# Optimization experiments

Measured on AMD Instinct MI355X. Metric: run time of the kernel, lower is better.

Reference implementation:

```python
import jax, jax.numpy as jnp
import numpy as np


def _dense_image_warp(image, flow):
    """Faithful JAX port of tfa.image.dense_image_warp.

    image: [B,H,W,C] float, flow: [B,H,W,2] float (flow[...,0]=dy, flow[...,1]=dx).
    query point (y,x) = grid(y,x) - flow; bilinear interp with TFA's clamping:
    floor clipped to [0, size-2], alpha clipped to [0,1].
    """
    B, H, W, C = image.shape
    gy, gx = jnp.meshgrid(
        jnp.arange(H, dtype=flow.dtype), jnp.arange(W, dtype=flow.dtype), indexing="ij"
    )
    qy = gy[None] - flow[..., 0]  # [B,H,W]
    qx = gx[None] - flow[..., 1]

    y0f = jnp.clip(jnp.floor(qy), 0.0, H - 2)
    x0f = jnp.clip(jnp.floor(qx), 0.0, W - 2)
    ay = jnp.clip(qy - y0f, 0.0, 1.0)[..., None]  # [B,H,W,1]
    ax = jnp.clip(qx - x0f, 0.0, 1.0)[..., None]

    y0 = y0f.astype(jnp.int32)
    x0 = x0f.astype(jnp.int32)
    b = jnp.arange(B, dtype=jnp.int32)[:, None, None]

    tl = image[b, y0, x0]          # top-left  [B,H,W,C]
    tr = image[b, y0, x0 + 1]      # top-right
    bl = image[b, y0 + 1, x0]      # bottom-left
    br = image[b, y0 + 1, x0 + 1]  # bottom-right

    top = tl + ax * (tr - tl)
    bot = bl + ax * (br - bl)
    return top + ay * (bot - top)


def setup_inputs() -> dict:
    key = jax.random.key(0)
    k1, k2 = jax.random.split(key)
    B, H, W, C = 8, 1024, 768, 3
    image = jax.random.normal(k1, (B, H, W, C), dtype=jnp.float32)
    # flow magnitudes of a few pixels, typical for appearance-flow warping
    flow = jax.random.normal(k2, (B, H, W, 2), dtype=jnp.float32) * 5.0
    return {"image": image, "flow": flow}


def reference(image, flow):
    return _dense_image_warp(image, flow)
```

## Files before the change

### kernel.cpp

```cpp
#include <hip/hip_runtime.h>


constexpr int B = 8;
constexpr int H = 1024;
constexpr int W = 768;
constexpr int C = 3;

constexpr int TY = 32, TX = 32;
constexpr int WIN_ROWS = 65;
constexpr int WIN_COLS = 64;
constexpr int WSTRIDE = WIN_COLS * C;
constexpr int CHUNKS  = WIN_ROWS * (WSTRIDE / 4);
constexpr int TILES_X = W / TX;
constexpr int TILES_Y = H / TY;
constexpr int TILES_PER_B = TILES_X * TILES_Y;

constexpr int NTHREADS = 512;
constexpr int PX_PER_T = (TY * TX) / NTHREADS;

typedef float vfloat2 __attribute__((ext_vector_type(2)));
typedef float vfloat4 __attribute__((ext_vector_type(4)));
typedef float vfloat2_a4 __attribute__((ext_vector_type(2), aligned(4)));
typedef float vfloat4_a4 __attribute__((ext_vector_type(4), aligned(4)));

__global__ __launch_bounds__(NTHREADS, 6) void warp_kernel(
    const float* __restrict__ image,
    const float* __restrict__ flow,
    float* __restrict__ out)
{
    __shared__ float win[WIN_ROWS * WSTRIDE + 64];

    const int flat = blockIdx.x;
    const int b    = flat & 7;
    const int s    = flat >> 3;
    const int ty   = s / TILES_X;
    const int tx   = s - ty * TILES_X;
    const int Y0 = ty * TY, X0 = tx * TX;

    const int rowLo = min(max(Y0 - 16, 0), H - WIN_ROWS);
    const int colLo = min(max((X0 - 15) & ~3, 0), W - WIN_COLS);

    const int lane = threadIdx.x & 63;
    const int wv   = threadIdx.x >> 6;

    const float* gwin = image + ((size_t)b * H + rowLo) * (W * C) + colLo * C;
#pragma unroll 1
    for (int j = wv; j * 64 < CHUNKS; j += 8) {
        int ci = j * 64 + lane;
        if (ci >= CHUNKS) ci = CHUNKS - 1;
        const int r = ci / 48;
        const int c = ci - r * 48;
        const float* g = gwin + (size_t)r * (W * C) + c * 4;
        __builtin_amdgcn_global_load_lds(
            (const __attribute__((address_space(1))) void*)g,
            (__attribute__((address_space(3))) void*)(win + (size_t)j * 256),
            16, 0, 0);
    }

    vfloat2 f[PX_PER_T];
#pragma unroll
    for (int k = 0; k < PX_PER_T; ++k) {
        const int p   = threadIdx.x + k * NTHREADS;
        const int py  = p >> 5;
        const int pxx = p & 31;
        const size_t pix = ((size_t)b * H + (Y0 + py)) * W + (X0 + pxx);
        f[k] = __builtin_nontemporal_load((const vfloat2*)flow + pix);
    }

    __syncthreads();

#pragma unroll
    for (int k = 0; k < PX_PER_T; ++k) {
        const int p   = threadIdx.x + k * NTHREADS;
        const int py  = p >> 5;
        const int pxx = p & 31;
        const int y = Y0 + py;
        const int x = X0 + pxx;
        const size_t pix = ((size_t)b * H + y) * W + x;

        const float qy = (float)y - f[k].x;
        const float qx = (float)x - f[k].y;

        float y0f = floorf(qy);
        float x0f = floorf(qx);
        y0f = fminf(fmaxf(y0f, 0.0f), (float)(H - 2));
        x0f = fminf(fmaxf(x0f, 0.0f), (float)(W - 2));
        const float ay = fminf(fmaxf(qy - y0f, 0.0f), 1.0f);
        const float ax = fminf(fmaxf(qx - x0f, 0.0f), 1.0f);

        const int y0 = (int)y0f;
        const int x0 = (int)x0f;

        float tl0, tl1, tl2, tr0, tr1, tr2, bl0, bl1, bl2, br0, br1, br2;

        const bool inwin = (y0 >= rowLo) & (y0 <= rowLo + WIN_ROWS - 2) &
                           (x0 >= colLo) & (x0 <= colLo + WIN_COLS - 2);
        if (inwin) {
            const float* t = &win[(y0 - rowLo) * WSTRIDE + (x0 - colLo) * C];
            tl0 = t[0]; tl1 = t[1]; tl2 = t[2];
            tr0 = t[3]; tr1 = t[4]; tr2 = t[5];
            const float* bo = t + WSTRIDE;
            bl0 = bo[0]; bl1 = bo[1]; bl2 = bo[2];
            br0 = bo[3]; br1 = bo[4]; br2 = bo[5];
        } else {
            const float* top = image + (((size_t)b * H + y0) * W + x0) * C;
            const float* bot = top + (size_t)W * C;
            const vfloat4 t4 = *(const vfloat4_a4*)top;
            const vfloat2 t2 = *(const vfloat2_a4*)(top + 4);
            const vfloat4 b4 = *(const vfloat4_a4*)bot;
            const vfloat2 b2 = *(const vfloat2_a4*)(bot + 4);
            tl0 = t4.x; tl1 = t4.y; tl2 = t4.z;
            tr0 = t4.w; tr1 = t2.x; tr2 = t2.y;
            bl0 = b4.x; bl1 = b4.y; bl2 = b4.z;
            br0 = b4.w; br1 = b2.x; br2 = b2.y;
        }

        const float tp0 = tl0 + ax * (tr0 - tl0);
        const float tp1 = tl1 + ax * (tr1 - tl1);
        const float tp2 = tl2 + ax * (tr2 - tl2);
        const float bo0 = bl0 + ax * (br0 - bl0);
        const float bo1 = bl1 + ax * (br1 - bl1);
        const float bo2 = bl2 + ax * (br2 - bl2);

        float* o = out + pix * C;
        __builtin_nontemporal_store(tp0 + ay * (bo0 - tp0), &o[0]);
        __builtin_nontemporal_store(tp1 + ay * (bo1 - tp1), &o[1]);
        __builtin_nontemporal_store(tp2 + ay * (bo2 - tp2), &o[2]);
    }
}

extern "C" void kernel_launch(void* const* d_in, const int* in_sizes, int n_in,
                              void* d_out, int out_size, void* d_ws, size_t ws_size,
                              hipStream_t stream) {
    const float* image = (const float*)d_in[0];
    const float* flow  = (const float*)d_in[1];
    float* out = (float*)d_out;

    dim3 grid(B * TILES_PER_B);
    dim3 block(NTHREADS);
    warp_kernel<<<grid, block, 0, stream>>>(image, flow, out);
}
```

Baseline: 176.1 us.

## Store LDS window as one float4 per pixel for aligned vector gathers

Changes the shared-memory window layout from packed RGB floats to one 16-byte slot per pixel. Each lane's global_load_lds pulls 16 bytes starting at a pixel, so the gather becomes four aligned ds_read_b128 loads instead of twelve scalar reads. LDS use grows to 64 KB per block and the occupancy hint drops from 6 to 4 blocks. Global loads now overlap, since each 12-byte pixel is fetched as 16 bytes, and the window is one column narrower, which slightly raises the chance of falling back to global memory.

```diff
diff --git a/kernel.cpp b/kernel.cpp
--- a/kernel.cpp
+++ b/kernel.cpp
@@ -8,14 +8,15 @@
 
 constexpr int TY = 32, TX = 32;
 constexpr int WIN_ROWS = 65;
-constexpr int WIN_COLS = 64;
-constexpr int WSTRIDE = WIN_COLS * C;
-constexpr int CHUNKS  = WIN_ROWS * (WSTRIDE / 4);
+constexpr int WIN_COLS = 63;
+constexpr int WIN_PX = WIN_ROWS * WIN_COLS;
 constexpr int TILES_X = W / TX;
 constexpr int TILES_Y = H / TY;
 constexpr int TILES_PER_B = TILES_X * TILES_Y;
 
 constexpr int NTHREADS = 512;
+constexpr int NWAVES = NTHREADS / 64;
+constexpr int ISSUES = (WIN_PX + 63) / 64;
 constexpr int PX_PER_T = (TY * TX) / NTHREADS;
 
 typedef float vfloat2 __attribute__((ext_vector_type(2)));
@@ -23,12 +24,12 @@
 typedef float vfloat2_a4 __attribute__((ext_vector_type(2), aligned(4)));
 typedef float vfloat4_a4 __attribute__((ext_vector_type(4), aligned(4)));
 
-__global__ __launch_bounds__(NTHREADS, 6) void warp_kernel(
+__global__ __launch_bounds__(NTHREADS, 4) void warp_kernel(
     const float* __restrict__ image,
     const float* __restrict__ flow,
     float* __restrict__ out)
 {
-    __shared__ float win[WIN_ROWS * WSTRIDE + 64];
+    __shared__ vfloat4 win4[4096];
 
     const int flat = blockIdx.x;
     const int b    = flat & 7;
@@ -38,22 +39,23 @@
     const int Y0 = ty * TY, X0 = tx * TX;
 
     const int rowLo = min(max(Y0 - 16, 0), H - WIN_ROWS);
-    const int colLo = min(max((X0 - 15) & ~3, 0), W - WIN_COLS);
+    const int colLo = min(max(X0 - 15, 0), W - WIN_COLS - 1);
 
     const int lane = threadIdx.x & 63;
     const int wv   = threadIdx.x >> 6;
 
     const float* gwin = image + ((size_t)b * H + rowLo) * (W * C) + colLo * C;
 #pragma unroll 1
-    for (int j = wv; j * 64 < CHUNKS; j += 8) {
+    for (int i = 0; i < ISSUES / NWAVES; ++i) {
+        const int j = i * NWAVES + wv;
         int ci = j * 64 + lane;
-        if (ci >= CHUNKS) ci = CHUNKS - 1;
-        const int r = ci / 48;
-        const int c = ci - r * 48;
-        const float* g = gwin + (size_t)r * (W * C) + c * 4;
+        if (ci > WIN_PX - 1) ci = WIN_PX - 1;
+        const int r = ci / WIN_COLS;
+        const int c = ci - r * WIN_COLS;
+        const float* g = gwin + (size_t)r * (W * C) + c * 3;
         __builtin_amdgcn_global_load_lds(
             (const __attribute__((address_space(1))) void*)g,
-            (__attribute__((address_space(3))) void*)(win + (size_t)j * 256),
+            (__attribute__((address_space(3))) void*)(win4 + (size_t)j * 64),
             16, 0, 0);
     }
 
@@ -96,12 +98,15 @@
         const bool inwin = (y0 >= rowLo) & (y0 <= rowLo + WIN_ROWS - 2) &
                            (x0 >= colLo) & (x0 <= colLo + WIN_COLS - 2);
         if (inwin) {
-            const float* t = &win[(y0 - rowLo) * WSTRIDE + (x0 - colLo) * C];
-            tl0 = t[0]; tl1 = t[1]; tl2 = t[2];
-            tr0 = t[3]; tr1 = t[4]; tr2 = t[5];
-            const float* bo = t + WSTRIDE;
-            bl0 = bo[0]; bl1 = bo[1]; bl2 = bo[2];
-            br0 = bo[3]; br1 = bo[4]; br2 = bo[5];
+            const int idx = (y0 - rowLo) * WIN_COLS + (x0 - colLo);
+            const vfloat4 tl = win4[idx];
+            const vfloat4 tr = win4[idx + 1];
+            const vfloat4 bl = win4[idx + WIN_COLS];
+            const vfloat4 br = win4[idx + WIN_COLS + 1];
+            tl0 = tl.x; tl1 = tl.y; tl2 = tl.z;
+            tr0 = tr.x; tr1 = tr.y; tr2 = tr.z;
+            bl0 = bl.x; bl1 = bl.y; bl2 = bl.z;
+            br0 = br.x; br1 = br.y; br2 = br.z;
         } else {
             const float* top = image + (((size_t)b * H + y0) * W + x0) * C;
             const float* bot = top + (size_t)W * C;
```

Measured after the change: 179.1 us. No clear change (+1.7%).
